# Kernel tuning notes

Measured on AMD Instinct MI355X. Metric: run time of the kernel, lower is better.

Reference implementation:

```python
import jax, jax.numpy as jnp
import numpy as np

# Static config (matches init_kwargs)
B, L, D = 4, 4096, 1024
K, H, M = 32, 32, 1           # key heads, per-head dim, num_thetas
A = 4                          # num_anchor_heads
CK = 4                         # conv_kernel_size (causal depthwise)
D_INNER = D                    # expand_factor = 1
ZC = 2 * D_INNER + K           # in_proj output channels = 2080
FLAT = K * H * M
SPLIT = H * M


def setup_inputs() -> dict:
    key = jax.random.key(0)
    ks = jax.random.split(key, 6)
    x = jax.random.normal(ks[0], (B, L, D), jnp.float32)
    # in_proj Dense(d_inner*2 + K, no bias): [D, ZC]
    W_in = jax.random.normal(ks[1], (D, ZC), jnp.float32) / np.sqrt(D)
    # depthwise causal conv kernel, flax 'WIO' layout: [CK, 1, ZC]
    conv_kernel = jax.random.normal(ks[2], (CK, 1, ZC), jnp.float32) / np.sqrt(CK)
    # theta init for M == 1: linspace grid with alternating signs
    grid = np.linspace(0.1, 1.5, K * H).reshape(1, 1, K, H, 1)
    signs = np.resize([1.0, -1.0], grid.shape)
    theta = jnp.asarray(grid * signs, jnp.float32)
    # inverse-softplus of geomspace slopes
    decay_slopes = jnp.asarray(np.log(np.exp(np.geomspace(0.001, 0.1, K - A)) - 1.0), jnp.float32)
    anchor_slopes = jnp.asarray(np.log(np.exp(np.geomspace(0.01, 0.1, A)) - 1.0), jnp.float32)
    score_scale = jnp.ones((K,), jnp.float32)
    lim = float(np.sqrt(6.0 / (SPLIT + H)))  # glorot uniform
    W_re = jax.random.uniform(ks[3], (SPLIT, H), jnp.float32, -lim, lim)
    W_im = jax.random.uniform(ks[4], (SPLIT, H), jnp.float32, -lim, lim)
    norm_scale = jnp.ones((2 * SPLIT,), jnp.float32)
    W_out = jax.random.normal(ks[5], (D_INNER, D), jnp.float32) / np.sqrt(D_INNER)
    return {"x": x, "W_in": W_in, "conv_kernel": conv_kernel, "theta": theta,
            "decay_slopes": decay_slopes, "anchor_slopes": anchor_slopes,
            "score_scale": score_scale, "W_re": W_re, "W_im": W_im,
            "norm_scale": norm_scale, "W_out": W_out}


def reference(x, W_in, conv_kernel, theta, decay_slopes, anchor_slopes,
              score_scale, W_re, W_im, norm_scale, W_out):
    b, l, _ = x.shape
    z = x @ W_in                                           # [b,l,ZC]
    # causal depthwise conv (padding (CK-1, 0), groups == channels)
    z = jax.lax.conv_general_dilated(
        z, conv_kernel, window_strides=(1,), padding=((CK - 1, 0),),
        dimension_numbers=('NWC', 'WIO', 'NWC'), feature_group_count=ZC)
    x_val = z[..., :D_INNER].reshape(b, l, K, H)
    x_gate = jax.nn.silu(z[..., D_INNER:2 * D_INNER])      # [b,l,d_inner]
    s_raw = z[..., -K:].reshape(b, l, K, 1)
    # ALiBi-style log time weights: decay heads look back, anchor heads decay from start
    pos = jnp.arange(l, dtype=jnp.float32)
    dist = jnp.maximum(jnp.float32(l - 1) - pos, 0.0)      # maxlen=None -> l
    log_w = jnp.concatenate([
        -jax.nn.softplus(decay_slopes).reshape(1, 1, -1, 1) * dist[None, :, None, None],
        -jax.nn.softplus(anchor_slopes).reshape(1, 1, -1, 1) * pos[None, :, None, None],
    ], axis=2)                                             # [1,l,K,1]
    p_w = jnp.exp(score_scale[None, None, :, None] * s_raw + log_w)  # [b,l,K,1]
    # complex phase features
    phi = x_val[..., None] * theta                         # [b,l,K,H,M]
    pwb = p_w[..., None]
    num_re_in = (pwb * jnp.cos(phi)).reshape(b, l, FLAT)
    num_im_in = (pwb * jnp.sin(phi)).reshape(b, l, FLAT)
    merged = jnp.concatenate([p_w.squeeze(-1), num_re_in, num_im_in], axis=-1)
    cs = jnp.cumsum(merged, axis=1)                        # causal prefix sum over seq
    den, num_re, num_im = jnp.split(cs, [K, K + FLAT], axis=-1)
    inv_den = 1.0 / jnp.maximum(den.reshape(b, l, K, 1), 1e-4)
    re = num_re.reshape(b, l, K, SPLIT) * inv_den
    im = num_im.reshape(b, l, K, SPLIT) * inv_den
    # running RMS normalization over complex features
    mean_sq = (jnp.sum(re * re, -1) + jnp.sum(im * im, -1)) / (2 * SPLIT)
    rs = jax.lax.rsqrt(mean_sq[..., None] + 1e-5)
    y = (re * rs * norm_scale[:SPLIT]) @ W_re + (im * rs * norm_scale[SPLIT:]) @ W_im  # [b,l,K,H]
    return (y.reshape(b, l, D_INNER) * x_gate) @ W_out
```

## Files before the change

kernel.cpp:

```cpp
#include <hip/hip_runtime.h>
#include <hip/hip_bf16.h>
#include <math.h>

#define BB 4
#define LL 4096
#define DD 1024
#define KK 32
#define HH 32
#define AA 4
#define CKK 4
#define DI 1024
#define ZC 2080
#define FLATC 1024
#define BL (BB * LL)
#define ZLD 2080
#define NPAD 2176

#define CCH 32
#define NCHK (LL / CCH)

#define GLD 1136
#define KLD 1080
#define SGLD 1080

typedef unsigned short u16;
typedef __attribute__((ext_vector_type(8))) short s16x8;
typedef __attribute__((ext_vector_type(4))) float f32x4;

__device__ __forceinline__ u16 f2bf(float f) {
  union { float f; unsigned int u; } v; v.f = f;
  unsigned int r = (v.u + 0x7FFFu + ((v.u >> 16) & 1u)) >> 16;
  return (u16)r;
}
__device__ __forceinline__ float bf2f(u16 u) {
  union { unsigned int i; float f; } x; x.i = ((unsigned int)u) << 16; return x.f;
}
__device__ __forceinline__ void gl_lds16(const void* g, void* l) {
  __builtin_amdgcn_global_load_lds(
      (const __attribute__((address_space(1))) unsigned int*)g,
      (__attribute__((address_space(3))) unsigned int*)l, 16, 0, 0);
}

__global__ __launch_bounds__(256) void cast_bf16_kernel(
    const float* __restrict__ src, u16* __restrict__ dst, int n) {
  const int i = (blockIdx.x * 256 + threadIdx.x) * 8;
  if (i >= n) return;
  float4 a = *(const float4*)(src + i);
  float4 b = *(const float4*)(src + i + 4);
  s16x8 v;
  v[0] = (short)f2bf(a.x); v[1] = (short)f2bf(a.y);
  v[2] = (short)f2bf(a.z); v[3] = (short)f2bf(a.w);
  v[4] = (short)f2bf(b.x); v[5] = (short)f2bf(b.y);
  v[6] = (short)f2bf(b.z); v[7] = (short)f2bf(b.w);
  *(s16x8*)(dst + i) = v;
}

__global__ __launch_bounds__(256) void transpose_cast_kernel(
    const float* __restrict__ src, u16* __restrict__ dst,
    int R, int C, int Cpad) {
  __shared__ float t[32][33];
  const int tid = threadIdx.x;
  const int r0 = blockIdx.x * 32, c0 = blockIdx.y * 32;
  const int lr = tid >> 5, lc = tid & 31;
#pragma unroll
  for (int i = 0; i < 4; ++i) {
    const int r = r0 + i * 8 + lr, c = c0 + lc;
    float v = 0.f;
    if (r < R && c < C) v = src[(size_t)r * C + c];
    t[lc][i * 8 + lr] = v;
  }
  __syncthreads();
#pragma unroll
  for (int i = 0; i < 4; ++i) {
    const int dr = c0 + i * 8 + lr;
    const int dc = r0 + lc;
    if (dr < Cpad && dc < R) dst[(size_t)dr * R + dc] = f2bf(t[i * 8 + lr][lc]);
  }
}

#define FENCE() asm volatile("" ::: "memory")
#define SBAR() do { FENCE(); __builtin_amdgcn_s_barrier(); FENCE(); } while (0)
#define VMCNT6() asm volatile("s_waitcnt vmcnt(6)" ::: "memory")

#define RA(s, h) (((s) * 2 + (h)) * 8192)
#define RB(s, h) (32768 + ((s) * 2 + (h)) * 8192)

template <int OUT_BF16>
__global__ __launch_bounds__(512, 2) void gemm256_8ph(
    const u16* __restrict__ A, const u16* __restrict__ Bt, void* __restrict__ C,
    int lda, int ldb, int ldc, int Kd, int Ncols) {
  __shared__ u16 lds[65536];
  const int tid = threadIdx.x;
  const int lane = tid & 63, wv = tid >> 6;
  const int wm = wv >> 2, wn = wv & 3;
  const int lm = lane & 15, lq = lane >> 4;
  const int bm = blockIdx.x * 256, bn = blockIdx.y * 256;
  const int NT = Kd >> 6;
  const int NT2 = NT >> 1;

  const int rofs = wv * 8 + (lane >> 3);
  const int cel = ((lane & 7) ^ (lane >> 3)) * 8;

  auto stageH = [&](const u16* __restrict__ G, int rowBase, int ld, int kt,
                    int regU16) {
    const u16* g0 = G + (size_t)(rowBase + rofs) * ld + (kt << 6) + cel;
    gl_lds16(g0, &lds[regU16 + wv * 512]);
    const u16* g1 = G + (size_t)(rowBase + 64 + rofs) * ld + (kt << 6) + cel;
    gl_lds16(g1, &lds[regU16 + 4096 + wv * 512]);
  };

  s16x8 Af[4][2], Bf[4][2];
  f32x4 acc[8][4];
  const f32x4 z4 = {0.f, 0.f, 0.f, 0.f};
#pragma unroll
  for (int i = 0; i < 8; ++i)
#pragma unroll
    for (int j = 0; j < 4; ++j) acc[i][j] = z4;

  const int xorw = (lm & 7) << 3;

#define DSA(s, mh)                                                          \
  _Pragma("unroll") for (int f = 0; f < 4; ++f)                             \
  _Pragma("unroll") for (int ks = 0; ks < 2; ++ks)                          \
    Af[f][ks] = *(const s16x8*)&lds[RA(s, wm) +                             \
      (((((mh) * 4 + f) * 16 + lm) * 64 + ((ks * 32 + lq * 8) ^ xorw)))];

#define DSB(s)                                                              \
  _Pragma("unroll") for (int f = 0; f < 4; ++f)                             \
  _Pragma("unroll") for (int ks = 0; ks < 2; ++ks)                          \
    Bf[f][ks] = *(const s16x8*)&lds[RB(s, wn >> 1) +                        \
      ((((wn & 1) * 64 + f * 16 + lm) * 64 + ((ks * 32 + lq * 8) ^ xorw)))];

#define QUAD(mh, nh)                                                        \
  do {                                                                      \
    __builtin_amdgcn_s_setprio(1);                                          \
    _Pragma("unroll") for (int f = 0; f < 4; ++f)                           \
    _Pragma("unroll") for (int n = 0; n < 2; ++n)                           \
    _Pragma("unroll") for (int ks = 0; ks < 2; ++ks)                        \
      acc[(mh) * 4 + f][(nh) * 2 + n] =                                     \
          __builtin_amdgcn_mfma_f32_16x16x32_bf16(                          \
              Af[f][ks], Bf[(nh) * 2 + n][ks],                              \
              acc[(mh) * 4 + f][(nh) * 2 + n], 0, 0, 0);                    \
    __builtin_amdgcn_s_setprio(0);                                          \
  } while (0)

  stageH(A, bm, lda, 0, RA(0, 0));
  stageH(A, bm + 128, lda, 0, RA(0, 1));
  stageH(Bt, bn, ldb, 0, RB(0, 0));
  stageH(Bt, bn + 128, ldb, 0, RB(0, 1));
  stageH(Bt, bn, ldb, 1, RB(1, 0));
  stageH(Bt, bn + 128, ldb, 1, RB(1, 1));
  stageH(A, bm, lda, 1, RA(1, 0));
  VMCNT6();
  SBAR();

#pragma unroll 1
  for (int t = 0; t < NT2; ++t) {
    const int T2 = 2 * t + 2, T3 = 2 * t + 3;
    DSA(0, 0); DSB(0);
    stageH(A, bm + 128, lda, 2 * t + 1, RA(1, 1));
    SBAR();
    QUAD(0, 0);
    SBAR();
    if (T2 < NT) stageH(Bt, bn, ldb, T2, RB(0, 0));
    SBAR();
    QUAD(0, 1);
    SBAR();
    DSA(0, 1);
    if (T2 < NT) stageH(Bt, bn + 128, ldb, T2, RB(0, 1));
    SBAR();
    QUAD(1, 0);
    SBAR();
    if (T2 < NT) stageH(A, bm, lda, T2, RA(0, 0));
    SBAR();
    QUAD(1, 1);
    VMCNT6();
    SBAR();
    DSA(1, 0); DSB(1);
    if (T2 < NT) stageH(A, bm + 128, lda, T2, RA(0, 1));
    SBAR();
    QUAD(0, 0);
    SBAR();
    if (T3 < NT) stageH(Bt, bn, ldb, T3, RB(1, 0));
    SBAR();
    QUAD(0, 1);
    SBAR();
    DSA(1, 1);
    if (T3 < NT) stageH(Bt, bn + 128, ldb, T3, RB(1, 1));
    SBAR();
    QUAD(1, 0);
    SBAR();
    if (T3 < NT) stageH(A, bm, lda, T3, RA(1, 0));
    SBAR();
    QUAD(1, 1);
    VMCNT6();
    SBAR();
  }

#pragma unroll
  for (int f = 0; f < 8; ++f) {
#pragma unroll
    for (int n = 0; n < 4; ++n) {
#pragma unroll
      for (int r = 0; r < 4; ++r) {
        const int row = bm + wm * 128 + f * 16 + lq * 4 + r;
        const int col = bn + wn * 64 + n * 16 + lm;
        if (col < Ncols) {
          if (OUT_BF16)
            ((u16*)C)[(size_t)row * ldc + col] = f2bf(acc[f][n][r]);
          else
            ((float*)C)[(size_t)row * ldc + col] = acc[f][n][r];
        }
      }
    }
  }
#undef DSA
#undef DSB
#undef QUAD
}

__global__ __launch_bounds__(256) void score_gemm(
    const u16* __restrict__ A, const u16* __restrict__ Bt,
    u16* __restrict__ z) {
  __shared__ u16 As[8192];
  __shared__ u16 Bs[2048];
  const int tid = threadIdx.x;
  const int lane = tid & 63, wv = tid >> 6;
  const int lm = lane & 15, lq = lane >> 4;
  const int bm = blockIdx.x * 128;

  const f32x4 z4 = {0.f, 0.f, 0.f, 0.f};
  f32x4 acc[2][2];
#pragma unroll
  for (int i = 0; i < 2; ++i)
#pragma unroll
    for (int j = 0; j < 2; ++j) acc[i][j] = z4;

  for (int k0 = 0; k0 < DD; k0 += 64) {
    __syncthreads();
#pragma unroll
    for (int t = 0; t < 5; ++t) {
      const int idx = wv * 5 + t;
      if (idx < 16) {
        const int mt = idx >> 1, kt = idx & 1;
        const u16* g = A + (size_t)(bm + mt * 16 + lm) * DD + k0 + kt * 32 + lq * 8;
        gl_lds16(g, &As[idx * 512]);
      } else {
        const int bidx = idx - 16;
        const int nt = bidx >> 1, kt = bidx & 1;
        const u16* g = Bt + (size_t)(2048 + nt * 16 + lm) * DD + k0 + kt * 32 + lq * 8;
        gl_lds16(g, &Bs[bidx * 512]);
      }
    }
    __syncthreads();
#pragma unroll
    for (int kt = 0; kt < 2; ++kt) {
      s16x8 af[2], bfb[2];
#pragma unroll
      for (int i = 0; i < 2; ++i) {
        const int mt = wv * 2 + i;
        af[i] = *(const s16x8*)&As[(mt * 2 + kt) * 512 + lane * 8];
        bfb[i] = *(const s16x8*)&Bs[(i * 2 + kt) * 512 + lane * 8];
      }
#pragma unroll
      for (int i = 0; i < 2; ++i)
#pragma unroll
        for (int j = 0; j < 2; ++j)
          acc[i][j] = __builtin_amdgcn_mfma_f32_16x16x32_bf16(af[i], bfb[j], acc[i][j], 0, 0, 0);
    }
  }
#pragma unroll
  for (int i = 0; i < 2; ++i)
#pragma unroll
    for (int j = 0; j < 2; ++j)
#pragma unroll
      for (int r = 0; r < 4; ++r) {
        const int row = bm + wv * 32 + i * 16 + lq * 4 + r;
        const int col = 2048 + j * 16 + lm;
        z[(size_t)row * ZLD + col] = f2bf(acc[i][j][r]);
      }
}

__global__ __launch_bounds__(256) void conv_feat_scan(
    const u16* __restrict__ z, const float* __restrict__ kern,
    const float* __restrict__ theta, const float* __restrict__ decay,
    const float* __restrict__ anchor, const float* __restrict__ sscale,
    float* __restrict__ merged, float* __restrict__ part) {
  __shared__ float pbuf[CCH][KK];
  __shared__ u16 zt[35 * 256];
  const int tid = threadIdx.x;
  const int r0 = blockIdx.x * CCH;
  const bool first = ((r0 & (LL - 1)) == 0);
  const int chunk = blockIdx.x;

#pragma unroll
  for (int q = 0; q < 4; ++q) {
    const int item = q * 256 + tid;
    const int row = item >> 5, k = item & 31;
    float v = 0.f;
#pragma unroll
    for (int w = 0; w < CKK; ++w) {
      const int g = row + w;
      float zv = 0.f;
      if (!(first && g < 3))
        zv = bf2f(z[(size_t)(r0 - 3 + g) * ZLD + 2048 + k]);
      v = fmaf(zv, kern[w * ZC + 2048 + k], v);
    }
    const int l = (r0 + row) & (LL - 1);
    const float slope = (k < KK - AA) ? decay[k] : anchor[k - (KK - AA)];
    const float sp = log1pf(__expf(slope));
    const float lw = (k < KK - AA) ? (-sp * (float)(LL - 1 - l)) : (-sp * (float)l);
    pbuf[row][k] = __expf(sscale[k] * v + lw);
  }
  __syncthreads();

  if (tid < KK) {
    float run = 0.f;
#pragma unroll
    for (int row = 0; row < CCH; ++row) {
      run += pbuf[row][tid];
      merged[(size_t)(r0 + row) * ZC + tid] = run;
    }
    part[(size_t)chunk * ZC + tid] = run;
  }

#pragma unroll 1
  for (int it = 0; it < 4; ++it) {
    __syncthreads();
    for (int u = tid; u < 35 * 32; u += 256) {
      const int row = u >> 5, q8 = (u & 31) * 8;
      s16x8 v = {0, 0, 0, 0, 0, 0, 0, 0};
      if (!(first && row < 3))
        v = *(const s16x8*)(z + (size_t)(r0 - 3 + row) * ZLD + it * 256 + q8);
      *(s16x8*)&zt[row * 256 + q8] = v;
    }
    __syncthreads();

    const int c = it * 256 + tid;
    const float kw0 = kern[0 * ZC + c], kw1 = kern[1 * ZC + c];
    const float kw2 = kern[2 * ZC + c], kw3 = kern[3 * ZC + c];
    const float th = theta[c];
    const int head = c >> 5;
    float h0 = bf2f(zt[0 * 256 + tid]);
    float h1 = bf2f(zt[1 * 256 + tid]);
    float h2 = bf2f(zt[2 * 256 + tid]);
    float sre = 0.f, sim = 0.f;
#pragma unroll 4
    for (int row = 0; row < CCH; ++row) {
      const float h3 = bf2f(zt[(row + 3) * 256 + tid]);
      float v = h0 * kw0;
      v = fmaf(h1, kw1, v);
      v = fmaf(h2, kw2, v);
      v = fmaf(h3, kw3, v);
      h0 = h1; h1 = h2; h2 = h3;
      const float phi = v * th;
      float sv, cv;
      __sincosf(phi, &sv, &cv);
      const float p = pbuf[row][head];
      sre = fmaf(p, cv, sre);
      sim = fmaf(p, sv, sim);
      float* mrow = merged + (size_t)(r0 + row) * ZC;
      mrow[KK + c] = sre;
      mrow[KK + FLATC + c] = sim;
    }
    part[(size_t)chunk * ZC + KK + c] = sre;
    part[(size_t)chunk * ZC + KK + FLATC + c] = sim;
  }
}

__global__ __launch_bounds__(256) void scan_offsets_kernel(float* __restrict__ part) {
  const int c = blockIdx.x * 256 + threadIdx.x;
  const int b = blockIdx.z;
  if (c >= ZC) return;
  float run = 0.f;
#pragma unroll 8
  for (int i = 0; i < NCHK; ++i) {
    const size_t idx = ((size_t)b * NCHK + i) * ZC + c;
    const float t = part[idx];
    part[idx] = run;
    run += t;
  }
}

__global__ __launch_bounds__(256) void wprime_kernel(
    const float* __restrict__ W_re, const float* __restrict__ W_im,
    const float* __restrict__ ns, u16* __restrict__ wp) {
  const int i = blockIdx.x * 256 + threadIdx.x;
  if (i < 1024) wp[i] = f2bf(ns[i >> 5] * W_re[i]);
  else {
    const int j = i - 1024;
    wp[i] = f2bf(ns[32 + (j >> 5)] * W_im[j]);
  }
}

__global__ __launch_bounds__(256) void norm_head_mfma(
    float* merged, const u16* __restrict__ z, const float* __restrict__ kern,
    const u16* __restrict__ wp, const float* __restrict__ part) {
  __shared__ __align__(16) char smem[42272];
  u16* zw = (u16*)smem;
  float* skern = (float*)(smem + 24992);
  float* sgf = (float*)smem;
  const int tid = threadIdx.x;
  const int r0 = blockIdx.x * 8;
  const bool first = ((r0 & (LL - 1)) == 0);
  const int lane = tid & 63, wv = tid >> 6;
  const int lm = lane & 15, lq = lane >> 4;
  const float* po = part + (size_t)(blockIdx.x >> 2) * ZC;

  for (int idx = tid; idx < 11 * 128; idx += 256) {
    const int i = idx >> 7, c8 = idx & 127;
    s16x8 v = {0, 0, 0, 0, 0, 0, 0, 0};
    if (!(first && i < 3))
      v = *(const s16x8*)(z + (size_t)(r0 - 3 + i) * ZLD + 1024 + c8 * 8);
    *(s16x8*)&zw[i * GLD + c8 * 8 + (c8 >> 4) * 16] = v;
  }
  for (int idx = tid; idx < 4 * 256; idx += 256) {
    const int w = idx >> 8, c4 = idx & 255;
    float4 v = *(const float4*)(kern + w * ZC + 1024 + c4 * 4);
    *(float4*)&skern[w * KLD + c4 * 4 + (c4 >> 5) * 8] = v;
  }

  s16x8 bre[2], bim[2];
#pragma unroll
  for (int nt = 0; nt < 2; ++nt)
#pragma unroll
    for (int jj = 0; jj < 8; ++jj) {
      bre[nt][jj] = (short)wp[(lq * 8 + jj) * 32 + nt * 16 + lm];
      bim[nt][jj] = (short)wp[1024 + (lq * 8 + jj) * 32 + nt * 16 + lm];
    }
  __syncthreads();

  const int rh = tid >> 7;
  const int cb = (tid & 127) * 8;
  float gbuf[4][8];
  {
    const int sc = cb + (cb >> 7) * 8;
    const int szb = cb + (cb >> 7) * 16;
#pragma unroll
    for (int j = 0; j < 4; ++j) {
      const int rr = rh * 4 + j;
      float gv[8] = {0.f, 0.f, 0.f, 0.f, 0.f, 0.f, 0.f, 0.f};
#pragma unroll
      for (int w_ = 0; w_ < 4; ++w_) {
        s16x8 zv = *(const s16x8*)&zw[(rr + w_) * GLD + szb];
        float4 ka = *(const float4*)&skern[w_ * KLD + sc];
        float4 kb = *(const float4*)&skern[w_ * KLD + sc + 4];
        gv[0] = fmaf(bf2f((u16)zv[0]), ka.x, gv[0]);
        gv[1] = fmaf(bf2f((u16)zv[1]), ka.y, gv[1]);
        gv[2] = fmaf(bf2f((u16)zv[2]), ka.z, gv[2]);
        gv[3] = fmaf(bf2f((u16)zv[3]), ka.w, gv[3]);
        gv[4] = fmaf(bf2f((u16)zv[4]), kb.x, gv[4]);
        gv[5] = fmaf(bf2f((u16)zv[5]), kb.y, gv[5]);
        gv[6] = fmaf(bf2f((u16)zv[6]), kb.z, gv[6]);
        gv[7] = fmaf(bf2f((u16)zv[7]), kb.w, gv[7]);
      }
#pragma unroll
      for (int e = 0; e < 8; ++e)
        gbuf[j][e] = gv[e] * (1.0f / (1.0f + __expf(-gv[e])));
    }
  }
  __syncthreads();
  {
    const int sgc = cb + (cb >> 7) * 8;
#pragma unroll
    for (int j = 0; j < 4; ++j) {
      float4 a = {gbuf[j][0], gbuf[j][1], gbuf[j][2], gbuf[j][3]};
      float4 b = {gbuf[j][4], gbuf[j][5], gbuf[j][6], gbuf[j][7]};
      *(float4*)&sgf[(rh * 4 + j) * SGLD + sgc] = a;
      *(float4*)&sgf[(rh * 4 + j) * SGLD + sgc + 4] = b;
    }
  }
  __syncthreads();

  const f32x4 z4 = {0.f, 0.f, 0.f, 0.f};
#pragma unroll 1
  for (int rr2 = 0; rr2 < 2; ++rr2) {
    const int rr = wv * 2 + rr2;
    const int bl = r0 + rr;
    float* row = merged + (size_t)bl * ZC;
    const float den0 = row[lm] + po[lm];
    const float den1 = row[16 + lm] + po[16 + lm];

#pragma unroll
    for (int khalf = 0; khalf < 2; ++khalf) {
      const int co = KK + (khalf * 16 + lm) * 32 + lq * 8;
      const float* rp = row + co;
      const float* pp = po + co;
      float4 ra = *(const float4*)rp;
      float4 rb = *(const float4*)(rp + 4);
      float4 ia = *(const float4*)(rp + FLATC);
      float4 ib = *(const float4*)(rp + FLATC + 4);
      float4 qa = *(const float4*)pp;
      float4 qb = *(const float4*)(pp + 4);
      float4 ja = *(const float4*)(pp + FLATC);
      float4 jb = *(const float4*)(pp + FLATC + 4);
      ra.x += qa.x; ra.y += qa.y; ra.z += qa.z; ra.w += qa.w;
      rb.x += qb.x; rb.y += qb.y; rb.z += qb.z; rb.w += qb.w;
      ia.x += ja.x; ia.y += ja.y; ia.z += ja.z; ia.w += ja.w;
      ib.x += jb.x; ib.y += jb.y; ib.z += jb.z; ib.w += jb.w;

      float ssq = ra.x * ra.x + ra.y * ra.y + ra.z * ra.z + ra.w * ra.w +
                  rb.x * rb.x + rb.y * rb.y + rb.z * rb.z + rb.w * rb.w +
                  ia.x * ia.x + ia.y * ia.y + ia.z * ia.z + ia.w * ia.w +
                  ib.x * ib.x + ib.y * ib.y + ib.z * ib.z + ib.w * ib.w;
      ssq += __shfl_xor(ssq, 16);
      ssq += __shfl_xor(ssq, 32);
      const float den = khalf ? den1 : den0;
      const float inv = 1.0f / fmaxf(den, 1e-4f);
      const float scale = inv * rsqrtf(ssq * inv * inv * (1.0f / 64.0f) + 1e-5f);

      s16x8 afr, afi;
      afr[0] = (short)f2bf(ra.x * scale); afr[1] = (short)f2bf(ra.y * scale);
      afr[2] = (short)f2bf(ra.z * scale); afr[3] = (short)f2bf(ra.w * scale);
      afr[4] = (short)f2bf(rb.x * scale); afr[5] = (short)f2bf(rb.y * scale);
      afr[6] = (short)f2bf(rb.z * scale); afr[7] = (short)f2bf(rb.w * scale);
      afi[0] = (short)f2bf(ia.x * scale); afi[1] = (short)f2bf(ia.y * scale);
      afi[2] = (short)f2bf(ia.z * scale); afi[3] = (short)f2bf(ia.w * scale);
      afi[4] = (short)f2bf(ib.x * scale); afi[5] = (short)f2bf(ib.y * scale);
      afi[6] = (short)f2bf(ib.z * scale); afi[7] = (short)f2bf(ib.w * scale);

      f32x4 acc[2];
#pragma unroll
      for (int nt = 0; nt < 2; ++nt) {
        acc[nt] = __builtin_amdgcn_mfma_f32_16x16x32_bf16(afr, bre[nt], z4, 0, 0, 0);
        acc[nt] = __builtin_amdgcn_mfma_f32_16x16x32_bf16(afi, bim[nt], acc[nt], 0, 0, 0);
      }

      u16* grow = (u16*)row;
#pragma unroll
      for (int nt = 0; nt < 2; ++nt) {
#pragma unroll
        for (int r = 0; r < 4; ++r) {
          const int k = khalf * 16 + lq * 4 + r;
          const int o = k * 32 + nt * 16 + lm;
          const float sil = sgf[rr * SGLD + o + (o >> 7) * 8];
          grow[o] = f2bf(acc[nt][r] * sil);
        }
      }
    }
  }
}

extern "C" void kernel_launch(void* const* d_in, const int* in_sizes, int n_in,
                              void* d_out, int out_size, void* d_ws, size_t ws_size,
                              hipStream_t stream) {
  const float* x      = (const float*)d_in[0];
  const float* W_in   = (const float*)d_in[1];
  const float* kern   = (const float*)d_in[2];
  const float* theta  = (const float*)d_in[3];
  const float* decay  = (const float*)d_in[4];
  const float* anchor = (const float*)d_in[5];
  const float* sscale = (const float*)d_in[6];
  const float* W_re   = (const float*)d_in[7];
  const float* W_im   = (const float*)d_in[8];
  const float* nscale = (const float*)d_in[9];
  const float* W_out  = (const float*)d_in[10];
  float* out = (float*)d_out;

  char* w = (char*)d_ws;
  float* merged = (float*)w;
  u16* xbf = (u16*)w;
  u16* zbf = (u16*)(w + (size_t)BL * ZC * 4);
  u16* wobt = zbf;
  u16* wp = (u16*)(w + (size_t)BL * ZC * 4 + (size_t)BL * ZLD * 2);
  u16* wbt = wp + 2048;
  float* part = (float*)wbt;

  cast_bf16_kernel<<<dim3(BL * DD / 8 / 256), 256, 0, stream>>>(x, xbf, BL * DD);
  transpose_cast_kernel<<<dim3(32, 68), 256, 0, stream>>>(W_in, wbt, DD, ZC, NPAD);
  wprime_kernel<<<dim3(8), 256, 0, stream>>>(W_re, W_im, nscale, wp);

  score_gemm<<<dim3(BL / 128), 256, 0, stream>>>(xbf, wbt, zbf);

  gemm256_8ph<1><<<dim3(BL / 256, 8), 512, 0, stream>>>(
      xbf, wbt, zbf, DD, DD, ZLD, DD, ZC);

  conv_feat_scan<<<dim3(BL / CCH), 256, 0, stream>>>(
      zbf, kern, theta, decay, anchor, sscale, merged, part);

  {
    dim3 grid2((ZC + 255) / 256, 1, BB);
    scan_offsets_kernel<<<grid2, 256, 0, stream>>>(part);
  }

  norm_head_mfma<<<dim3(BL / 8), 256, 0, stream>>>(merged, zbf, kern, wp, part);

  transpose_cast_kernel<<<dim3(32, 32), 256, 0, stream>>>(W_out, wobt, DI, DD, DD);
  gemm256_8ph<0><<<dim3(BL / 256, DD / 256), 512, 0, stream>>>(
      (const u16*)merged, wobt, out, 2 * ZC, DI, DD, DI, DD);
}
```

Before: 361.0 us.

## Store chunk-local scan features in bf16 and fuse prep kernels into one launch

The conv/feature scan now writes its chunk-local prefix sums as bf16 into a dense 2048-wide buffer, with denominators in a separate small fp32 buffer, instead of fp32 into a 2080-wide merged array. norm_head reads the bf16 data, adds the fp32 chunk offsets, and writes the gated output to its own compact buffer, which the output GEMM reads with stride 1024. The four preprocessing kernels (x cast, both weight transposes and the W_re/W_im prep) are merged into one launch. The aim is to roughly halve the memory traffic of the largest intermediate and cut launch overhead, at the cost of bf16 rounding on the partial cumulative sums.

New measurement: 349.1 us. -3.3%, faster.

```diff
diff --git a/kernel.cpp b/kernel.cpp
--- a/kernel.cpp
+++ b/kernel.cpp
@@ -41,26 +41,46 @@
       (__attribute__((address_space(3))) unsigned int*)l, 16, 0, 0);
 }
 
-__global__ __launch_bounds__(256) void cast_bf16_kernel(
-    const float* __restrict__ src, u16* __restrict__ dst, int n) {
-  const int i = (blockIdx.x * 256 + threadIdx.x) * 8;
-  if (i >= n) return;
-  float4 a = *(const float4*)(src + i);
-  float4 b = *(const float4*)(src + i + 4);
-  s16x8 v;
-  v[0] = (short)f2bf(a.x); v[1] = (short)f2bf(a.y);
-  v[2] = (short)f2bf(a.z); v[3] = (short)f2bf(a.w);
-  v[4] = (short)f2bf(b.x); v[5] = (short)f2bf(b.y);
-  v[6] = (short)f2bf(b.z); v[7] = (short)f2bf(b.w);
-  *(s16x8*)(dst + i) = v;
-}
-
-__global__ __launch_bounds__(256) void transpose_cast_kernel(
-    const float* __restrict__ src, u16* __restrict__ dst,
-    int R, int C, int Cpad) {
+__global__ __launch_bounds__(256) void prep_kernel(
+    const float* __restrict__ x, u16* __restrict__ xbf,
+    const float* __restrict__ W_in, u16* __restrict__ wbt,
+    const float* __restrict__ W_out, u16* __restrict__ wobt,
+    const float* __restrict__ W_re, const float* __restrict__ W_im,
+    const float* __restrict__ ns, u16* __restrict__ wp) {
   __shared__ float t[32][33];
+  const int bid = blockIdx.x;
   const int tid = threadIdx.x;
-  const int r0 = blockIdx.x * 32, c0 = blockIdx.y * 32;
+  if (bid < 8192) {
+    const int i = (bid * 256 + tid) * 8;
+    float4 a = *(const float4*)(x + i);
+    float4 b = *(const float4*)(x + i + 4);
+    s16x8 v;
+    v[0] = (short)f2bf(a.x); v[1] = (short)f2bf(a.y);
+    v[2] = (short)f2bf(a.z); v[3] = (short)f2bf(a.w);
+    v[4] = (short)f2bf(b.x); v[5] = (short)f2bf(b.y);
+    v[6] = (short)f2bf(b.z); v[7] = (short)f2bf(b.w);
+    *(s16x8*)(xbf + i) = v;
+    return;
+  }
+  if (bid >= 8192 + 2176 + 1024) {
+    const int i = (bid - (8192 + 2176 + 1024)) * 256 + tid;
+    if (i < 1024) wp[i] = f2bf(ns[i >> 5] * W_re[i]);
+    else {
+      const int j = i - 1024;
+      wp[i] = f2bf(ns[32 + (j >> 5)] * W_im[j]);
+    }
+    return;
+  }
+  const float* src; u16* dst; int R, C, Cpad, r0, c0;
+  if (bid < 8192 + 2176) {
+    const int id = bid - 8192;
+    src = W_in; dst = wbt; R = DD; C = ZC; Cpad = NPAD;
+    r0 = (id & 31) * 32; c0 = (id >> 5) * 32;
+  } else {
+    const int id = bid - (8192 + 2176);
+    src = W_out; dst = wobt; R = DI; C = DD; Cpad = DD;
+    r0 = (id & 31) * 32; c0 = (id >> 5) * 32;
+  }
   const int lr = tid >> 5, lc = tid & 31;
 #pragma unroll
   for (int i = 0; i < 4; ++i) {
@@ -285,7 +305,8 @@
     const u16* __restrict__ z, const float* __restrict__ kern,
     const float* __restrict__ theta, const float* __restrict__ decay,
     const float* __restrict__ anchor, const float* __restrict__ sscale,
-    float* __restrict__ merged, float* __restrict__ part) {
+    u16* __restrict__ mbf, float* __restrict__ dbuf,
+    float* __restrict__ part) {
   __shared__ float pbuf[CCH][KK];
   __shared__ u16 zt[35 * 256];
   const int tid = threadIdx.x;
@@ -319,7 +340,7 @@
 #pragma unroll
     for (int row = 0; row < CCH; ++row) {
       run += pbuf[row][tid];
-      merged[(size_t)(r0 + row) * ZC + tid] = run;
+      dbuf[(size_t)(r0 + row) * KK + tid] = run;
     }
     part[(size_t)chunk * ZC + tid] = run;
   }
@@ -359,9 +380,9 @@
       const float p = pbuf[row][head];
       sre = fmaf(p, cv, sre);
       sim = fmaf(p, sv, sim);
-      float* mrow = merged + (size_t)(r0 + row) * ZC;
-      mrow[KK + c] = sre;
-      mrow[KK + FLATC + c] = sim;
+      u16* mrow = mbf + (size_t)(r0 + row) * 2048;
+      mrow[c] = f2bf(sre);
+      mrow[1024 + c] = f2bf(sim);
     }
     part[(size_t)chunk * ZC + KK + c] = sre;
     part[(size_t)chunk * ZC + KK + FLATC + c] = sim;
@@ -382,20 +403,11 @@
   }
 }
 
-__global__ __launch_bounds__(256) void wprime_kernel(
-    const float* __restrict__ W_re, const float* __restrict__ W_im,
-    const float* __restrict__ ns, u16* __restrict__ wp) {
-  const int i = blockIdx.x * 256 + threadIdx.x;
-  if (i < 1024) wp[i] = f2bf(ns[i >> 5] * W_re[i]);
-  else {
-    const int j = i - 1024;
-    wp[i] = f2bf(ns[32 + (j >> 5)] * W_im[j]);
-  }
-}
-
 __global__ __launch_bounds__(256) void norm_head_mfma(
-    float* merged, const u16* __restrict__ z, const float* __restrict__ kern,
-    const u16* __restrict__ wp, const float* __restrict__ part) {
+    const u16* __restrict__ mbf, const float* __restrict__ dbuf,
+    const u16* __restrict__ z, const float* __restrict__ kern,
+    const u16* __restrict__ wp, const float* __restrict__ part,
+    u16* __restrict__ g) {
   __shared__ __align__(16) char smem[42272];
   u16* zw = (u16*)smem;
   float* skern = (float*)(smem + 24992);
@@ -477,32 +489,37 @@
   for (int rr2 = 0; rr2 < 2; ++rr2) {
     const int rr = wv * 2 + rr2;
     const int bl = r0 + rr;
-    float* row = merged + (size_t)bl * ZC;
-    const float den0 = row[lm] + po[lm];
-    const float den1 = row[16 + lm] + po[16 + lm];
+    const float* dd = dbuf + (size_t)bl * KK;
+    const float den0 = dd[lm] + po[lm];
+    const float den1 = dd[16 + lm] + po[16 + lm];
 
 #pragma unroll
     for (int khalf = 0; khalf < 2; ++khalf) {
-      const int co = KK + (khalf * 16 + lm) * 32 + lq * 8;
-      const float* rp = row + co;
-      const float* pp = po + co;
-      float4 ra = *(const float4*)rp;
-      float4 rb = *(const float4*)(rp + 4);
-      float4 ia = *(const float4*)(rp + FLATC);
-      float4 ib = *(const float4*)(rp + FLATC + 4);
+      const int co = (khalf * 16 + lm) * 32 + lq * 8;
+      const u16* rp = mbf + (size_t)bl * 2048 + co;
+      s16x8 vre = *(const s16x8*)rp;
+      s16x8 vim = *(const s16x8*)(rp + 1024);
+      const float* pp = po + KK + co;
       float4 qa = *(const float4*)pp;
       float4 qb = *(const float4*)(pp + 4);
       float4 ja = *(const float4*)(pp + FLATC);
       float4 jb = *(const float4*)(pp + FLATC + 4);
-      ra.x += qa.x; ra.y += qa.y; ra.z += qa.z; ra.w += qa.w;
-      rb.x += qb.x; rb.y += qb.y; rb.z += qb.z; rb.w += qb.w;
-      ia.x += ja.x; ia.y += ja.y; ia.z += ja.z; ia.w += ja.w;
-      ib.x += jb.x; ib.y += jb.y; ib.z += jb.z; ib.w += jb.w;
-
-      float ssq = ra.x * ra.x + ra.y * ra.y + ra.z * ra.z + ra.w * ra.w +
-                  rb.x * rb.x + rb.y * rb.y + rb.z * rb.z + rb.w * rb.w +
-                  ia.x * ia.x + ia.y * ia.y + ia.z * ia.z + ia.w * ia.w +
-                  ib.x * ib.x + ib.y * ib.y + ib.z * ib.z + ib.w * ib.w;
+      float re[8], im[8];
+      re[0] = bf2f((u16)vre[0]) + qa.x; re[1] = bf2f((u16)vre[1]) + qa.y;
+      re[2] = bf2f((u16)vre[2]) + qa.z; re[3] = bf2f((u16)vre[3]) + qa.w;
+      re[4] = bf2f((u16)vre[4]) + qb.x; re[5] = bf2f((u16)vre[5]) + qb.y;
+      re[6] = bf2f((u16)vre[6]) + qb.z; re[7] = bf2f((u16)vre[7]) + qb.w;
+      im[0] = bf2f((u16)vim[0]) + ja.x; im[1] = bf2f((u16)vim[1]) + ja.y;
+      im[2] = bf2f((u16)vim[2]) + ja.z; im[3] = bf2f((u16)vim[3]) + ja.w;
+      im[4] = bf2f((u16)vim[4]) + jb.x; im[5] = bf2f((u16)vim[5]) + jb.y;
+      im[6] = bf2f((u16)vim[6]) + jb.z; im[7] = bf2f((u16)vim[7]) + jb.w;
+
+      float ssq = 0.f;
+#pragma unroll
+      for (int e = 0; e < 8; ++e) {
+        ssq = fmaf(re[e], re[e], ssq);
+        ssq = fmaf(im[e], im[e], ssq);
+      }
       ssq += __shfl_xor(ssq, 16);
       ssq += __shfl_xor(ssq, 32);
       const float den = khalf ? den1 : den0;
@@ -510,14 +527,11 @@
       const float scale = inv * rsqrtf(ssq * inv * inv * (1.0f / 64.0f) + 1e-5f);
 
       s16x8 afr, afi;
-      afr[0] = (short)f2bf(ra.x * scale); afr[1] = (short)f2bf(ra.y * scale);
-      afr[2] = (short)f2bf(ra.z * scale); afr[3] = (short)f2bf(ra.w * scale);
-      afr[4] = (short)f2bf(rb.x * scale); afr[5] = (short)f2bf(rb.y * scale);
-      afr[6] = (short)f2bf(rb.z * scale); afr[7] = (short)f2bf(rb.w * scale);
-      afi[0] = (short)f2bf(ia.x * scale); afi[1] = (short)f2bf(ia.y * scale);
-      afi[2] = (short)f2bf(ia.z * scale); afi[3] = (short)f2bf(ia.w * scale);
-      afi[4] = (short)f2bf(ib.x * scale); afi[5] = (short)f2bf(ib.y * scale);
-      afi[6] = (short)f2bf(ib.z * scale); afi[7] = (short)f2bf(ib.w * scale);
+#pragma unroll
+      for (int e = 0; e < 8; ++e) {
+        afr[e] = (short)f2bf(re[e] * scale);
+        afi[e] = (short)f2bf(im[e] * scale);
+      }
 
       f32x4 acc[2];
 #pragma unroll
@@ -526,7 +540,7 @@
         acc[nt] = __builtin_amdgcn_mfma_f32_16x16x32_bf16(afi, bim[nt], acc[nt], 0, 0, 0);
       }
 
-      u16* grow = (u16*)row;
+      u16* grow = g + (size_t)bl * 1024;
 #pragma unroll
       for (int nt = 0; nt < 2; ++nt) {
 #pragma unroll
@@ -558,17 +572,18 @@
   float* out = (float*)d_out;
 
   char* w = (char*)d_ws;
-  float* merged = (float*)w;
-  u16* xbf = (u16*)w;
-  u16* zbf = (u16*)(w + (size_t)BL * ZC * 4);
-  u16* wobt = zbf;
-  u16* wp = (u16*)(w + (size_t)BL * ZC * 4 + (size_t)BL * ZLD * 2);
-  u16* wbt = wp + 2048;
-  float* part = (float*)wbt;
-
-  cast_bf16_kernel<<<dim3(BL * DD / 8 / 256), 256, 0, stream>>>(x, xbf, BL * DD);
-  transpose_cast_kernel<<<dim3(32, 68), 256, 0, stream>>>(W_in, wbt, DD, ZC, NPAD);
-  wprime_kernel<<<dim3(8), 256, 0, stream>>>(W_re, W_im, nscale, wp);
+  u16* mbf   = (u16*)w;
+  u16* xbf   = (u16*)w;
+  u16* zbf   = (u16*)(w + 67108864ull);
+  float* dbuf = (float*)(w + 135266304ull);
+  float* part = (float*)(w + 137363456ull);
+  u16* wp    = (u16*)(w + 141623296ull);
+  u16* wbt   = (u16*)(w + 141627392ull);
+  u16* g     = (u16*)(w + 146083840ull);
+  u16* wobt  = (u16*)(w + 179638272ull);
+
+  prep_kernel<<<dim3(8192 + 2176 + 1024 + 8), 256, 0, stream>>>(
+      x, xbf, W_in, wbt, W_out, wobt, W_re, W_im, nscale, wp);
 
   score_gemm<<<dim3(BL / 128), 256, 0, stream>>>(xbf, wbt, zbf);
 
@@ -576,16 +591,16 @@
       xbf, wbt, zbf, DD, DD, ZLD, DD, ZC);
 
   conv_feat_scan<<<dim3(BL / CCH), 256, 0, stream>>>(
-      zbf, kern, theta, decay, anchor, sscale, merged, part);
+      zbf, kern, theta, decay, anchor, sscale, mbf, dbuf, part);
 
   {
     dim3 grid2((ZC + 255) / 256, 1, BB);
     scan_offsets_kernel<<<grid2, 256, 0, stream>>>(part);
   }
 
-  norm_head_mfma<<<dim3(BL / 8), 256, 0, stream>>>(merged, zbf, kern, wp, part);
-
-  transpose_cast_kernel<<<dim3(32, 32), 256, 0, stream>>>(W_out, wobt, DI, DD, DD);
+  norm_head_mfma<<<dim3(BL / 8), 256, 0, stream>>>(
+      mbf, dbuf, zbf, kern, wp, part, g);
+
   gemm256_8ph<0><<<dim3(BL / 256, DD / 256), 512, 0, stream>>>(
-      (const u16*)merged, wobt, out, 2 * ZC, DI, DD, DI, DD);
-}
+      g, wobt, out, 1024, DD, DD, DI, DD);
+}
```
